# Kernel tuning notes

Hardware: AMD Instinct MI355X
Metric: run time of the kernel (lower is better)

## Reference

```python
import jax, jax.numpy as jnp
import numpy as np
import math

N, C, T, V = 8, 256, 128, 25
H, HC = 8, 32            # num_heads, head_channels
W, DIL = 3, 1            # window, dilation
O = 256                  # out_channels
PAD = (W + (W - 1) * (DIL - 1) - 1) // 2
B, L = N * T, W * V


def _ln(x, g, b):
    m = jnp.mean(x, -1, keepdims=True)
    v = jnp.var(x, -1, keepdims=True)
    return (x - m) * jax.lax.rsqrt(v + 1e-5) * g + b


def setup_inputs() -> dict:
    key = jax.random.key(0)
    ks = iter(jax.random.split(key, 40))
    def w(shape):
        return jax.random.normal(next(ks), shape, jnp.float32) * 0.02
    d = {"x": jax.random.normal(next(ks), (N, C, T, V), jnp.float32)}
    d.update(
        ln1_g=jnp.ones((C,)), ln1_b=jnp.zeros((C,)),
        Wq=w((C, C)), bq=jnp.zeros((C,)), Wqa=w((C, H)), bqa=jnp.zeros((H,)),
        Wk=w((C, C)), bk=jnp.zeros((C,)), Wka=w((C, H)), bka=jnp.zeros((H,)),
        Wv=w((C, C)), bv=jnp.zeros((C,)), Wt=w((C, C)), bt=jnp.zeros((C,)),
        Wp=w((C, C)), bp=jnp.zeros((C,)),
        ffn_g=jnp.ones((C,)), ffn_b=jnp.zeros((C,)),
        W1=w((C, C)), b1=jnp.zeros((C,)), W2=w((C, C)), b2=jnp.zeros((C,)),
        tn_g=jnp.ones((C,)), tn_b=jnp.zeros((C,)),
        c1_w=w((C, O)), c1_b=jnp.zeros((O,)),
        c2_w=w((W, O, O)), c2_b=jnp.zeros((O,)),
    )
    return d


def reference(x, ln1_g, ln1_b, Wq, bq, Wqa, bqa, Wk, bk, Wka, bka, Wv, bv,
              Wt, bt, Wp, bp, ffn_g, ffn_b, W1, b1, W2, b2, tn_g, tn_b,
              c1_w, c1_b, c2_w, c2_b):
    scale = 1.0 / math.sqrt(HC)
    # ---- Unfold over time: build window of frames around each t (nn.Unfold) ----
    xp = jnp.pad(x, ((0, 0), (0, 0), (PAD, PAD), (0, 0)))
    win = jnp.stack([jax.lax.dynamic_slice_in_dim(xp, k * DIL, T, 2) for k in range(W)], 2)  # (N,C,W,T,V)
    seq = win.transpose(0, 3, 2, 4, 1).reshape(B, L, C)  # (N*T, W*V, C)

    sep = lambda z: z.reshape(B, L, H, HC).transpose(0, 2, 1, 3)  # (B,H,L,HC)
    grp = lambda z: z.transpose(0, 2, 1, 3).reshape(B, -1, C)

    # ---- SpatioTemporalAttention (eval: dropouts off) ----
    nx = _ln(seq, ln1_g, ln1_b)
    q = nx @ Wq + bq                                            # (B,L,C)
    qw = jax.nn.softmax((q @ Wqa + bqa).transpose(0, 2, 1) * scale, axis=-1)  # (B,H,L)
    pq = jnp.einsum('bhl,bhlc->bhc', qw, sep(q)).reshape(B, 1, C)             # pooled query
    keys = nx @ Wk + bk
    kw = jax.nn.softmax(((keys * pq) @ Wka + bka).transpose(0, 2, 1) * scale, axis=-1)
    pk = jnp.einsum('bhl,bhlc->bhc', kw, sep(keys))             # pooled key (B,H,HC)
    vals = sep(nx @ Wv + bv)
    kv = grp(vals * pk[:, :, None, :]) @ Wt + bt                # (B,L,C)
    attn = (kv + q) @ Wp + bp                                   # residual-in-heads == plain add

    # ---- AttentionBranch residual + FFN ----
    att = attn + seq
    f = _ln(att, ffn_g, ffn_b)
    y = jax.nn.gelu(f @ W1 + b1, approximate=False) @ W2 + b2 + att  # (B,L,C)

    # ---- temporal branch: LN -> regroup frames -> 1x1 conv -> GELU -> (W,1) conv stride W ----
    t5 = _ln(y, tn_g, tn_b).reshape(N, T, W, V, C)
    h = jax.nn.gelu(t5 @ c1_w + c1_b, approximate=False)        # (N,T,W,V,O)
    out = jnp.einsum('ntwvi,wio->ntvo', h, c2_w) + c2_b         # stride==kernel conv == window contraction
    return out.transpose(0, 3, 1, 2)                            # (N,O,T,V)
```

## Files before the change

### kernel.cpp

```cpp
#include <hip/hip_runtime.h>


#define DI __device__ __forceinline__

constexpr int CC   = 256;
constexpr int CL   = 75;
constexpr int CV   = 25;
constexpr int CT   = 128;
constexpr int TP   = 130;
constexpr int MPAD = 8 * TP * CV;
constexpr int MBL  = 1024 * CL;
constexpr int MOUT = 8 * CT * CV;
constexpr float SM_SCALE = 0.17677669529663687f;

typedef __bf16 bf16x8 __attribute__((ext_vector_type(8)));
typedef float f32x4 __attribute__((ext_vector_type(4)));

DI float bf2f(unsigned short u) { return __uint_as_float(((unsigned)u) << 16); }
DI float bf2f_lo(unsigned u) { return __uint_as_float(u << 16); }
DI float bf2f_hi(unsigned u) { return __uint_as_float(u & 0xffff0000u); }
DI unsigned short f2bf(float f) {
  unsigned u = __float_as_uint(f);
  u += 0x7fffu + ((u >> 16) & 1u);
  return (unsigned short)(u >> 16);
}
DI unsigned packbf(float a, float b) {
  return (unsigned)f2bf(a) | ((unsigned)f2bf(b) << 16);
}
DI float geluf(float x) { return 0.5f * x * (1.f + erff(x * 0.70710678118654752440f)); }

DI void gll16(const unsigned short* g, unsigned short* l) {
  __builtin_amdgcn_global_load_lds(
      (const __attribute__((address_space(1))) unsigned int*)g,
      (__attribute__((address_space(3))) unsigned int*)l, 16, 0, 0);
}

DI int arow(int r) {
  int b = r / CL;
  int l = r - b * CL;
  int w = l / CV;
  int v = l - w * CV;
  int t = b & (CT - 1);
  int n = b >> 7;
  return (n * TP + t + w) * CV + v;
}

__global__ __launch_bounds__(256) void k_transpose(const float* __restrict__ x,
                                                   unsigned short* __restrict__ xtp) {
  __shared__ float tile[32][33];
  const int n = blockIdx.z;
  const int c0 = blockIdx.x * 32;
  const int tv0 = blockIdx.y * 32;
  const int tx = threadIdx.x & 31, ty = threadIdx.x >> 5;
#pragma unroll
  for (int j = 0; j < 32; j += 8) {
    tile[ty + j][tx] = x[((size_t)(n * CC + c0 + ty + j)) * 3200 + tv0 + tx];
  }
  __syncthreads();
#pragma unroll
  for (int j = 0; j < 32; j += 8) {
    int tv = tv0 + ty + j;
    int st = tv / CV, v = tv - st * CV;
    size_t row = ((size_t)n * TP + st + 1) * CV + v;
    xtp[row * CC + c0 + tx] = f2bf(tile[tx][ty + j]);
  }
}

__global__ __launch_bounds__(256) void k_zero_pad(unsigned short* __restrict__ xtp) {
  int i = blockIdx.x * 256 + threadIdx.x;
  int c = i & 255;
  int rid = i >> 8;
  int n = rid / 50;
  int rem = rid - n * 50;
  int side = rem / 25;
  int v = rem - side * 25;
  size_t row = ((size_t)n * TP + side * (TP - 1)) * CV + v;
  xtp[row * CC + c] = 0;
}

struct TJobs {
  const float* src[10];
  unsigned short* dst[10];
  int stride[10];
  int off[10];
};
__global__ __launch_bounds__(256) void k_wtrans(TJobs J) {
  __shared__ float tile[32][33];
  const int j = blockIdx.z;
  const float* src = J.src[j];
  unsigned short* dst = J.dst[j];
  const int stride = J.stride[j], off = J.off[j];
  const int k0 = blockIdx.x * 32, n0 = blockIdx.y * 32;
  const int tx = threadIdx.x & 31, ty = threadIdx.x >> 5;
#pragma unroll
  for (int jj = 0; jj < 32; jj += 8)
    tile[ty + jj][tx] = src[(size_t)(k0 + ty + jj) * 256 + n0 + tx];
  __syncthreads();
#pragma unroll
  for (int jj = 0; jj < 32; jj += 8)
    dst[(size_t)(n0 + ty + jj) * stride + off + k0 + tx] = f2bf(tile[tx][ty + jj]);
}

__global__ __launch_bounds__(256) void k_wtwp(const float* __restrict__ Wt,
                                              const float* __restrict__ Wp,
                                              unsigned short* __restrict__ fused) {
  __shared__ float wrow[256];
  const int k = blockIdx.x, n = threadIdx.x;
  wrow[n] = Wt[(size_t)k * 256 + n];
  __syncthreads();
  float acc = 0.f;
  for (int j = 0; j < 256; ++j) acc = fmaf(wrow[j], Wp[(size_t)j * 256 + n], acc);
  fused[(size_t)n * 512 + k] = f2bf(acc);
}

__global__ __launch_bounds__(256) void k_bias2(const float* __restrict__ bt,
                                               const float* __restrict__ Wp,
                                               const float* __restrict__ bp,
                                               const float* __restrict__ bq,
                                               const float* __restrict__ bk,
                                               const float* __restrict__ bv,
                                               float* __restrict__ bias2,
                                               float* __restrict__ bias3) {
  const int n = threadIdx.x;
  float acc = bp[n];
  for (int j = 0; j < 256; ++j) acc = fmaf(bt[j], Wp[(size_t)j * 256 + n], acc);
  bias2[n] = acc;
  bias3[n] = bq[n];
  bias3[256 + n] = bk[n];
  bias3[512 + n] = bv[n];
}

__global__ __launch_bounds__(256) void k_ln4(const unsigned short* __restrict__ X,
                                             const float* __restrict__ g,
                                             const float* __restrict__ b,
                                             unsigned short* __restrict__ Y) {
  const int row = blockIdx.x * 4 + (threadIdx.x >> 6);
  const int lane = threadIdx.x & 63;
  const uint2 u = *(const uint2*)(X + (size_t)row * CC + lane * 4);
  const float x0 = bf2f_lo(u.x), x1 = bf2f_hi(u.x), x2 = bf2f_lo(u.y), x3 = bf2f_hi(u.y);
  float s = x0 + x1 + x2 + x3;
  float q = x0 * x0 + x1 * x1 + x2 * x2 + x3 * x3;
#pragma unroll
  for (int o = 32; o; o >>= 1) { s += __shfl_xor(s, o); q += __shfl_xor(q, o); }
  const float mean = s * (1.f / CC);
  const float var = q * (1.f / CC) - mean * mean;
  const float rs = rsqrtf(var + 1e-5f);
  const float4 g4 = *(const float4*)(g + lane * 4);
  const float4 b4 = *(const float4*)(b + lane * 4);
  uint2 o2;
  o2.x = packbf((x0 - mean) * rs * g4.x + b4.x, (x1 - mean) * rs * g4.y + b4.y);
  o2.y = packbf((x2 - mean) * rs * g4.z + b4.z, (x3 - mean) * rs * g4.w + b4.w);
  *(uint2*)(Y + (size_t)row * CC + lane * 4) = o2;
}

template <int AMODE, int EPI, int KD, bool MULTI>
__global__ __launch_bounds__(512) void k_mgemm(const unsigned short* __restrict__ A,
                                               const unsigned short* __restrict__ BwT,
                                               const float* __restrict__ bias,
                                               unsigned short* __restrict__ Cout,
                                               float* __restrict__ FOut,
                                               int M) {
  if constexpr (MULTI) {
    const int z = blockIdx.y;
    BwT += (size_t)z * (256 * 256);
    bias += z * 256;
    Cout += (size_t)z * MPAD * CC;
  }
  __shared__ unsigned short SH[20480];
  const int tid = threadIdx.x;
  const int lane = tid & 63;
  const int wid = tid >> 6;
  const int wm = wid >> 2, wn = wid & 3;
  const int r0 = blockIdx.x * 64;
  f32x4 acc[2][4] = {};

  const bool sa = tid < 256;
  const int rA = r0 + (tid >> 2);
  const int seg8 = (tid & 3) * 8;
  const bool valid = sa && (rA < M);
  int hrb = 0;
  if (valid && AMODE == 4) {
    const int nb = rA / 3200, rr = rA - nb * 3200;
    const int tq = rr / 25, vq = rr - tq * 25;
    hrb = (nb * CT + tq) * CL + vq;
  }

  auto loadA4 = [&](int k0) -> uint4 {
    uint4 u = make_uint4(0, 0, 0, 0);
    if (!valid) return u;
    const int w = k0 >> 8;
    u = *(const uint4*)(A + (size_t)(hrb + w * CV) * CC + (k0 & 255) + seg8);
    return u;
  };
  auto stageB = [&](int buf, int k0) {
    unsigned short* bs = SH + 4096 + buf * 8192;
#pragma unroll
    for (int pp = 0; pp < 2; ++pp) {
      const int s = tid + pp * 512;
      gll16(BwT + (size_t)(s >> 2) * KD + k0 + (s & 3) * 8, bs + s * 8);
    }
  };
  auto stageAg = [&](int buf, int k0) {
    if (valid) gll16(A + (size_t)rA * CC + k0 + seg8, SH + buf * 2048 + tid * 8);
  };

  stageB(0, 0);
  if constexpr (AMODE == 0) {
    stageAg(0, 0);
  } else {
    const uint4 a0 = loadA4(0);
    if (sa) *(uint4*)(SH + tid * 8) = a0;
  }
  __syncthreads();

  constexpr int NT = KD / 32;
  int cur = 0;
  for (int t = 0; t < NT; ++t) {
    const int nxt = cur ^ 1;
    const bool more = (t + 1 < NT);
    uint4 an;
    if (more) {
      stageB(nxt, (t + 1) * 32);
      if constexpr (AMODE == 0) stageAg(nxt, (t + 1) * 32);
      else an = loadA4((t + 1) * 32);
    }
    const unsigned short* as = SH + cur * 2048;
    const unsigned short* bs = SH + 4096 + cur * 8192;
    bf16x8 af[2], bfr[4];
#pragma unroll
    for (int mi = 0; mi < 2; ++mi)
      af[mi] = *(const bf16x8*)(as + (wm * 32 + mi * 16 + (lane & 15)) * 32 + (lane >> 4) * 8);
#pragma unroll
    for (int ni = 0; ni < 4; ++ni)
      bfr[ni] = *(const bf16x8*)(bs + (wn * 64 + ni * 16 + (lane & 15)) * 32 + (lane >> 4) * 8);
#pragma unroll
    for (int mi = 0; mi < 2; ++mi)
#pragma unroll
      for (int ni = 0; ni < 4; ++ni)
        acc[mi][ni] = __builtin_amdgcn_mfma_f32_16x16x32_bf16(af[mi], bfr[ni], acc[mi][ni], 0, 0, 0);
    if (more) {
      if constexpr (AMODE != 0) {
        if (sa) *(uint4*)(SH + nxt * 2048 + tid * 8) = an;
      }
      __syncthreads();
      cur = nxt;
    }
  }

  const int ln15 = lane & 15, lq = lane >> 4;
  if constexpr (EPI == 4) {
#pragma unroll
    for (int mi = 0; mi < 2; ++mi) {
#pragma unroll
      for (int ni = 0; ni < 4; ++ni) {
        const int col = wn * 64 + ni * 16 + ln15;
        const float bcol = bias[col];
        const int rbase = r0 + wm * 32 + mi * 16 + lq * 4;
        const int nb = rbase / 3200, rr = rbase - nb * 3200;
        float4 v;
        v.x = acc[mi][ni][0] + bcol;
        v.y = acc[mi][ni][1] + bcol;
        v.z = acc[mi][ni][2] + bcol;
        v.w = acc[mi][ni][3] + bcol;
        *(float4*)(FOut + (size_t)nb * 819200 + (size_t)col * 3200 + rr) = v;
      }
    }
  } else {
    constexpr int LDC = 260;
    __syncthreads();
#pragma unroll
    for (int mi = 0; mi < 2; ++mi) {
#pragma unroll
      for (int ni = 0; ni < 4; ++ni) {
        const int col = wn * 64 + ni * 16 + ln15;
        const float bcol = bias[col];
#pragma unroll
        for (int rg = 0; rg < 4; ++rg) {
          const int lrow = wm * 32 + mi * 16 + lq * 4 + rg;
          SH[lrow * LDC + col] = f2bf(acc[mi][ni][rg] + bcol);
        }
      }
    }
    __syncthreads();
#pragma unroll
    for (int i = 0; i < 4; ++i) {
      const int idx = tid + i * 512;
      const int row = idx >> 5, ch = idx & 31;
      const int gr = r0 + row;
      if (gr < M)
        *(uint4*)(Cout + (size_t)gr * CC + ch * 8) = *(const uint4*)&SH[row * LDC + ch * 8];
    }
  }
}

__global__ __launch_bounds__(512) void k_chain(
    const unsigned short* __restrict__ VP, const unsigned short* __restrict__ QP,
    const float* __restrict__ PK, const unsigned short* __restrict__ XTP,
    const unsigned short* __restrict__ fusedB, const float* __restrict__ bias2,
    const unsigned short* __restrict__ W1T, const float* __restrict__ b1,
    const unsigned short* __restrict__ W2T, const float* __restrict__ b2,
    const float* __restrict__ ffn_g, const float* __restrict__ ffn_b,
    const unsigned short* __restrict__ c1wT, const float* __restrict__ c1b,
    const float* __restrict__ tn_g, const float* __restrict__ tn_b,
    unsigned short* __restrict__ Hout) {
  constexpr int LDC = 264;
  __shared__ unsigned short SH[16896 + 4096 + 16384];
  unsigned short* ACT = SH;
  unsigned short* AS = SH + 16896;
  unsigned short* BS = SH + 16896 + 4096;
  const int tid = threadIdx.x;
  const int lane = tid & 63, wid = tid >> 6;
  const int wm = wid >> 2, wn = wid & 3;
  const int ln15 = lane & 15, lq = lane >> 4;
  const int r0 = blockIdx.x * 64;

  const bool sa = tid < 256;
  const int rA = r0 + (tid >> 2);
  const int seg8 = (tid & 3) * 8;
  int ar = 0, bb = 0;
  if (sa) { ar = arow(rA); bb = rA / CL; }

  auto stageB = [&](const unsigned short* BwT, int KD, int buf, int k0) {
    unsigned short* bs = BS + buf * 8192;
#pragma unroll
    for (int pp = 0; pp < 2; ++pp) {
      const int s = tid + pp * 512;
      gll16(BwT + (size_t)(s >> 2) * KD + k0 + (s & 3) * 8, bs + s * 8);
    }
  };
  auto loadA5 = [&](int k0) -> uint4 {
    uint4 u = make_uint4(0, 0, 0, 0);
    if (!sa) return u;
    if (k0 < 256) {
      const int kg = k0 + seg8;
      const uint4 t4 = *(const uint4*)(VP + (size_t)ar * CC + kg);
      const float* sv = PK + bb * CC + kg;
      const float4 s0 = *(const float4*)sv;
      const float4 s1 = *(const float4*)(sv + 4);
      u.x = packbf(bf2f_lo(t4.x) * s0.x, bf2f_hi(t4.x) * s0.y);
      u.y = packbf(bf2f_lo(t4.y) * s0.z, bf2f_hi(t4.y) * s0.w);
      u.z = packbf(bf2f_lo(t4.z) * s1.x, bf2f_hi(t4.z) * s1.y);
      u.w = packbf(bf2f_lo(t4.w) * s1.z, bf2f_hi(t4.w) * s1.w);
    } else {
      u = *(const uint4*)(QP + (size_t)ar * CC + (k0 - 256) + seg8);
    }
    return u;
  };
  auto ln_inplace = [&](const float* g, const float* b) {
    const float4 g4 = *(const float4*)(g + lane * 4);
    const float4 b4 = *(const float4*)(b + lane * 4);
#pragma unroll
    for (int rr = 0; rr < 8; ++rr) {
      const int row = wid * 8 + rr;
      const uint2 u = *(const uint2*)(ACT + row * LDC + lane * 4);
      const float x0 = bf2f_lo(u.x), x1 = bf2f_hi(u.x);
      const float x2 = bf2f_lo(u.y), x3 = bf2f_hi(u.y);
      float s = x0 + x1 + x2 + x3;
      float q = x0 * x0 + x1 * x1 + x2 * x2 + x3 * x3;
#pragma unroll
      for (int o = 32; o; o >>= 1) { s += __shfl_xor(s, o); q += __shfl_xor(q, o); }
      const float mean = s * (1.f / CC);
      const float var = q * (1.f / CC) - mean * mean;
      const float rs = rsqrtf(var + 1e-5f);
      uint2 o2;
      o2.x = packbf((x0 - mean) * rs * g4.x + b4.x, (x1 - mean) * rs * g4.y + b4.y);
      o2.y = packbf((x2 - mean) * rs * g4.z + b4.z, (x3 - mean) * rs * g4.w + b4.w);
      *(uint2*)(ACT + row * LDC + lane * 4) = o2;
    }
  };
  auto gemmACT = [&](const unsigned short* BwT, f32x4 (&a)[2][4]) {
    int c2 = 0;
    for (int t = 0; t < 8; ++t) {
      if (t + 1 < 8) stageB(BwT, 256, c2 ^ 1, (t + 1) * 32);
      bf16x8 af[2], bfr[4];
#pragma unroll
      for (int mi = 0; mi < 2; ++mi)
        af[mi] = *(const bf16x8*)(ACT + (wm * 32 + mi * 16 + ln15) * LDC + t * 32 + lq * 8);
#pragma unroll
      for (int ni = 0; ni < 4; ++ni)
        bfr[ni] = *(const bf16x8*)(BS + c2 * 8192 + (wn * 64 + ni * 16 + ln15) * 32 + lq * 8);
#pragma unroll
      for (int mi = 0; mi < 2; ++mi)
#pragma unroll
        for (int ni = 0; ni < 4; ++ni)
          a[mi][ni] = __builtin_amdgcn_mfma_f32_16x16x32_bf16(af[mi], bfr[ni], a[mi][ni], 0, 0, 0);
      if (t + 1 < 8) { __syncthreads(); c2 ^= 1; }
    }
  };

  f32x4 acc[2][4] = {};
  stageB(fusedB, 512, 0, 0);
  { uint4 a0 = loadA5(0); if (sa) *(uint4*)(AS + tid * 8) = a0; }
  __syncthreads();
  int cur = 0;
  for (int t = 0; t < 16; ++t) {
    const int nxt = cur ^ 1;
    const bool more = (t + 1 < 16);
    uint4 an;
    if (more) { stageB(fusedB, 512, nxt, (t + 1) * 32); an = loadA5((t + 1) * 32); }
    bf16x8 af[2], bfr[4];
#pragma unroll
    for (int mi = 0; mi < 2; ++mi)
      af[mi] = *(const bf16x8*)(AS + cur * 2048 + (wm * 32 + mi * 16 + ln15) * 32 + lq * 8);
#pragma unroll
    for (int ni = 0; ni < 4; ++ni)
      bfr[ni] = *(const bf16x8*)(BS + cur * 8192 + (wn * 64 + ni * 16 + ln15) * 32 + lq * 8);
#pragma unroll
    for (int mi = 0; mi < 2; ++mi)
#pragma unroll
      for (int ni = 0; ni < 4; ++ni)
        acc[mi][ni] = __builtin_amdgcn_mfma_f32_16x16x32_bf16(af[mi], bfr[ni], acc[mi][ni], 0, 0, 0);
    if (more) {
      if (sa) *(uint4*)(AS + nxt * 2048 + tid * 8) = an;
      __syncthreads();
      cur = nxt;
    }
  }
  f32x4 attres[2][4];
#pragma unroll
  for (int mi = 0; mi < 2; ++mi) {
#pragma unroll
    for (int ni = 0; ni < 4; ++ni) {
      const int col = wn * 64 + ni * 16 + ln15;
      const float bcol = bias2[col];
#pragma unroll
      for (int rg = 0; rg < 4; ++rg) {
        const int r = r0 + wm * 32 + mi * 16 + lq * 4 + rg;
        attres[mi][ni][rg] = acc[mi][ni][rg] + bcol + bf2f(XTP[(size_t)arow(r) * CC + col]);
      }
    }
  }
  stageB(W1T, 256, 0, 0);
#pragma unroll
  for (int mi = 0; mi < 2; ++mi)
#pragma unroll
    for (int ni = 0; ni < 4; ++ni) {
      const int col = wn * 64 + ni * 16 + ln15;
#pragma unroll
      for (int rg = 0; rg < 4; ++rg)
        ACT[(wm * 32 + mi * 16 + lq * 4 + rg) * LDC + col] = f2bf(attres[mi][ni][rg]);
    }
  __syncthreads();
  ln_inplace(ffn_g, ffn_b);
  __syncthreads();

  f32x4 acc2[2][4] = {};
  gemmACT(W1T, acc2);
  stageB(W2T, 256, 0, 0);
  __syncthreads();
#pragma unroll
  for (int mi = 0; mi < 2; ++mi)
#pragma unroll
    for (int ni = 0; ni < 4; ++ni) {
      const int col = wn * 64 + ni * 16 + ln15;
      const float bcol = b1[col];
#pragma unroll
      for (int rg = 0; rg < 4; ++rg)
        ACT[(wm * 32 + mi * 16 + lq * 4 + rg) * LDC + col] = f2bf(geluf(acc2[mi][ni][rg] + bcol));
    }
  __syncthreads();

  f32x4 acc3[2][4] = {};
  gemmACT(W2T, acc3);
  stageB(c1wT, 256, 0, 0);
  __syncthreads();
#pragma unroll
  for (int mi = 0; mi < 2; ++mi)
#pragma unroll
    for (int ni = 0; ni < 4; ++ni) {
      const int col = wn * 64 + ni * 16 + ln15;
      const float bcol = b2[col];
#pragma unroll
      for (int rg = 0; rg < 4; ++rg)
        ACT[(wm * 32 + mi * 16 + lq * 4 + rg) * LDC + col] =
            f2bf(acc3[mi][ni][rg] + bcol + attres[mi][ni][rg]);
    }
  __syncthreads();
  ln_inplace(tn_g, tn_b);
  __syncthreads();

  f32x4 acc4[2][4] = {};
  gemmACT(c1wT, acc4);
  __syncthreads();
#pragma unroll
  for (int mi = 0; mi < 2; ++mi)
#pragma unroll
    for (int ni = 0; ni < 4; ++ni) {
      const int col = wn * 64 + ni * 16 + ln15;
      const float bcol = c1b[col];
#pragma unroll
      for (int rg = 0; rg < 4; ++rg)
        ACT[(wm * 32 + mi * 16 + lq * 4 + rg) * LDC + col] = f2bf(geluf(acc4[mi][ni][rg] + bcol));
    }
  __syncthreads();
#pragma unroll
  for (int i = 0; i < 4; ++i) {
    const int idx = tid + i * 512;
    const int row = idx >> 5, ch = idx & 31;
    *(uint4*)(Hout + (size_t)(r0 + row) * CC + ch * 8) = *(const uint4*)&ACT[row * LDC + ch * 8];
  }
}

__global__ __launch_bounds__(256) void k_proj8(const unsigned short* __restrict__ SRC,
                                               const float* __restrict__ Wsm,
                                               const float* __restrict__ bsm,
                                               float* __restrict__ OUT) {
  const int r = blockIdx.x * 4 + (threadIdx.x >> 6);
  const int lane = threadIdx.x & 63;
  const int c = lane * 4;
  const uint2 u = *(const uint2*)(SRC + (size_t)r * CC + c);
  const float m0 = bf2f_lo(u.x), m1 = bf2f_hi(u.x), m2 = bf2f_lo(u.y), m3 = bf2f_hi(u.y);
  float p[8] = {};
#pragma unroll
  for (int j = 0; j < 4; ++j) {
    const float mj = (j == 0) ? m0 : (j == 1) ? m1 : (j == 2) ? m2 : m3;
#pragma unroll
    for (int h = 0; h < 8; ++h) p[h] += mj * Wsm[(c + j) * 8 + h];
  }
#pragma unroll
  for (int h = 0; h < 8; ++h) {
#pragma unroll
    for (int o = 32; o; o >>= 1) p[h] += __shfl_down(p[h], o);
  }
  if (lane == 0) {
#pragma unroll
    for (int h = 0; h < 8; ++h) OUT[(size_t)r * 8 + h] = p[h] + bsm[h];
  }
}

template <int SIDE>
__global__ __launch_bounds__(256) void k_attpool(const unsigned short* __restrict__ ROWS,
                                                 const float* __restrict__ QA,
                                                 const float* __restrict__ PQ,
                                                 const float* __restrict__ Wka,
                                                 const float* __restrict__ bka,
                                                 float* __restrict__ OUT) {
  __shared__ unsigned short rows[CL * CC];
  __shared__ float uu[(SIDE == 1) ? 8 * 258 : 8];
  __shared__ float lg[8 * 76];
  __shared__ float inv8[8];
  __shared__ int arl[CL];
  const int b = blockIdx.x;
  const int t = threadIdx.x;

  if (t < CL) arl[t] = arow(b * CL + t);
  __syncthreads();

  for (int i = t; i < CL * 32; i += 256) {
    const int r = i >> 5, seg = i & 31;
    gll16(ROWS + (size_t)arl[r] * CC + seg * 8, &rows[i * 8]);
  }
  if constexpr (SIDE == 0) {
    for (int i = t; i < CL * 2; i += 256) {
      const int l = i >> 1, q = i & 1;
      const float4 v = *(const float4*)(QA + (size_t)arl[l] * 8 + q * 4);
      lg[(q * 4 + 0) * 76 + l] = v.x * SM_SCALE;
      lg[(q * 4 + 1) * 76 + l] = v.y * SM_SCALE;
      lg[(q * 4 + 2) * 76 + l] = v.z * SM_SCALE;
      lg[(q * 4 + 3) * 76 + l] = v.w * SM_SCALE;
    }
  } else {
    for (int i = t; i < CC * 8; i += 256) {
      const int c = i >> 3, h = i & 7;
      uu[h * 258 + c] = PQ[(size_t)b * CC + c] * Wka[c * 8 + h];
    }
  }
  __syncthreads();

  if constexpr (SIDE == 1) {
    const int c0 = (t & 127) * 2;
    for (int i = t; i < CL * 8; i += 256) {
      const int h = i / CL, l = i - h * CL;
      float acc = bka[h];
#pragma unroll 4
      for (int jj = 0; jj < CC; jj += 2) {
        const int c = (c0 + jj) & 255;
        const unsigned pr = *(const unsigned*)&rows[l * CC + c];
        acc = fmaf(bf2f_lo(pr), uu[h * 258 + c], acc);
        acc = fmaf(bf2f_hi(pr), uu[h * 258 + c + 1], acc);
      }
      lg[h * 76 + l] = acc * SM_SCALE;
    }
    __syncthreads();
  }

  if (t < 8) {
    float m = -1e30f;
    for (int l = 0; l < CL; ++l) m = fmaxf(m, lg[t * 76 + l]);
    float s = 0.f;
    for (int l = 0; l < CL; ++l) {
      const float e = __expf(lg[t * 76 + l] - m);
      lg[t * 76 + l] = e;
      s += e;
    }
    inv8[t] = 1.f / s;
  }
  __syncthreads();

  {
    const int h = t >> 5;
    float acc = 0.f;
    for (int l = 0; l < CL; ++l) acc = fmaf(lg[h * 76 + l], bf2f(rows[l * CC + t]), acc);
    OUT[(size_t)b * CC + t] = acc * inv8[h];
  }
}

extern "C" void kernel_launch(void* const* d_in, const int* in_sizes, int n_in,
                              void* d_out, int out_size, void* d_ws, size_t ws_size,
                              hipStream_t stream) {
  const float* x = (const float*)d_in[0];
  const float* ln1_g = (const float*)d_in[1];
  const float* ln1_b = (const float*)d_in[2];
  const float* Wq = (const float*)d_in[3];
  const float* bq = (const float*)d_in[4];
  const float* Wqa = (const float*)d_in[5];
  const float* bqa = (const float*)d_in[6];
  const float* Wk = (const float*)d_in[7];
  const float* bk = (const float*)d_in[8];
  const float* Wka = (const float*)d_in[9];
  const float* bka = (const float*)d_in[10];
  const float* Wv = (const float*)d_in[11];
  const float* bv = (const float*)d_in[12];
  const float* Wt = (const float*)d_in[13];
  const float* bt = (const float*)d_in[14];
  const float* Wp = (const float*)d_in[15];
  const float* bp = (const float*)d_in[16];
  const float* ffn_g = (const float*)d_in[17];
  const float* ffn_b = (const float*)d_in[18];
  const float* W1 = (const float*)d_in[19];
  const float* b1 = (const float*)d_in[20];
  const float* W2 = (const float*)d_in[21];
  const float* b2 = (const float*)d_in[22];
  const float* tn_g = (const float*)d_in[23];
  const float* tn_b = (const float*)d_in[24];
  const float* c1w = (const float*)d_in[25];
  const float* c1b = (const float*)d_in[26];
  const float* c2w = (const float*)d_in[27];
  const float* c2b = (const float*)d_in[28];
  float* out = (float*)d_out;

  char* wp = (char*)d_ws;
  auto alloc = [&](size_t bytes) -> char* {
    char* p = wp;
    wp += (bytes + 255) & ~(size_t)255;
    return p;
  };
  unsigned short* XTP = (unsigned short*)alloc((size_t)MPAD * CC * 2);
  unsigned short* LNXP = (unsigned short*)alloc((size_t)MPAD * CC * 2);
  unsigned short* QKVP = (unsigned short*)alloc((size_t)3 * MPAD * CC * 2);
  unsigned short* QP = QKVP;
  unsigned short* KP = QKVP + (size_t)MPAD * CC;
  unsigned short* VP = QKVP + (size_t)2 * MPAD * CC;
  unsigned short* Hb = (unsigned short*)alloc((size_t)MBL * CC * 2);
  float* QA = (float*)alloc((size_t)MPAD * 8 * 4);
  float* PQ = (float*)alloc((size_t)1024 * CC * 4);
  float* PK = (float*)alloc((size_t)1024 * CC * 4);
  unsigned short* WqkvT = (unsigned short*)alloc((size_t)3 * 256 * 256 * 2);
  unsigned short* W1T = (unsigned short*)alloc(256 * 256 * 2);
  unsigned short* W2T = (unsigned short*)alloc(256 * 256 * 2);
  unsigned short* c1wT = (unsigned short*)alloc(256 * 256 * 2);
  unsigned short* c2wT = (unsigned short*)alloc(256 * 768 * 2);
  unsigned short* fusedB = (unsigned short*)alloc(256 * 512 * 2);
  float* bias2 = (float*)alloc(256 * 4);
  float* bias3 = (float*)alloc(768 * 4);

  TJobs J;
  const float* srcs[10] = {Wq, Wk, Wv, W1, W2, c1w, c2w, c2w + 65536, c2w + 131072, Wp};
  unsigned short* dsts[10] = {WqkvT, WqkvT + 65536, WqkvT + 131072, W1T, W2T, c1wT,
                              c2wT, c2wT, c2wT, fusedB};
  const int strides[10] = {256, 256, 256, 256, 256, 256, 768, 768, 768, 512};
  const int offs[10] = {0, 0, 0, 0, 0, 0, 0, 256, 512, 256};
  for (int i = 0; i < 10; ++i) {
    J.src[i] = srcs[i]; J.dst[i] = dsts[i]; J.stride[i] = strides[i]; J.off[i] = offs[i];
  }
  k_wtrans<<<dim3(8, 8, 10), 256, 0, stream>>>(J);
  k_wtwp<<<256, 256, 0, stream>>>(Wt, Wp, fusedB);
  k_bias2<<<1, 256, 0, stream>>>(bt, Wp, bp, bq, bk, bv, bias2, bias3);

  k_transpose<<<dim3(8, 100, 8), 256, 0, stream>>>(x, XTP);
  k_zero_pad<<<400, 256, 0, stream>>>(XTP);
  k_ln4<<<MPAD / 4, 256, 0, stream>>>(XTP, ln1_g, ln1_b, LNXP);

  const int gP = (MPAD + 63) / 64;
  const int gO = MOUT / 64;
  k_mgemm<0, 0, 256, true><<<dim3(gP, 3), 512, 0, stream>>>(
      LNXP, WqkvT, bias3, QKVP, nullptr, MPAD);

  k_proj8<<<MPAD / 4, 256, 0, stream>>>(QP, Wqa, bqa, QA);
  k_attpool<0><<<1024, 256, 0, stream>>>(QP, QA, nullptr, nullptr, nullptr, PQ);
  k_attpool<1><<<1024, 256, 0, stream>>>(KP, nullptr, PQ, Wka, bka, PK);

  k_chain<<<MBL / 64, 512, 0, stream>>>(VP, QP, PK, XTP, fusedB, bias2,
                                        W1T, b1, W2T, b2, ffn_g, ffn_b,
                                        c1wT, c1b, tn_g, tn_b, Hb);

  k_mgemm<4, 4, 768, false><<<gO, 512, 0, stream>>>(Hb, c2wT, c2b, nullptr, out, MOUT);
}
```

Before: 311.8 us.

## Fuse query head projection into attention pooling and tweak chain kernel epilogue

Removes the separate k_proj8 kernel and QA buffer by computing the query head logits (q @ Wqa + bqa) directly inside k_attpool<0>, using the same shared-memory dot-product path the key side already uses. In k_chain, the residual rows are precomputed into registers, the W1 staging is issued earlier, and the ACT store is merged into the residual loop. A launch-bounds occupancy hint of 4 is added. In exchange, attpool<0> now does redundant per-window projection work for overlapping padded rows, and the occupancy hint may force register spills.

Result: no change. 311.7 us (-0.0%).

```diff
diff --git a/kernel.cpp b/kernel.cpp
--- a/kernel.cpp
+++ b/kernel.cpp
@@ -293,7 +293,7 @@
   }
 }
 
-__global__ __launch_bounds__(512) void k_chain(
+__global__ __launch_bounds__(512, 4) void k_chain(
     const unsigned short* __restrict__ VP, const unsigned short* __restrict__ QP,
     const float* __restrict__ PK, const unsigned short* __restrict__ XTP,
     const unsigned short* __restrict__ fusedB, const float* __restrict__ bias2,
@@ -319,6 +319,10 @@
   const int seg8 = (tid & 3) * 8;
   int ar = 0, bb = 0;
   if (sa) { ar = arow(rA); bb = rA / CL; }
+  int xrow[8];
+#pragma unroll
+  for (int i = 0; i < 8; ++i)
+    xrow[i] = arow(r0 + wm * 32 + (i >> 2) * 16 + lq * 4 + (i & 3));
 
   auto stageB = [&](const unsigned short* BwT, int KD, int buf, int k0) {
     unsigned short* bs = BS + buf * 8192;
@@ -416,6 +420,7 @@
       cur = nxt;
     }
   }
+  stageB(W1T, 256, 0, 0);
   f32x4 attres[2][4];
 #pragma unroll
   for (int mi = 0; mi < 2; ++mi) {
@@ -425,21 +430,12 @@
       const float bcol = bias2[col];
 #pragma unroll
       for (int rg = 0; rg < 4; ++rg) {
-        const int r = r0 + wm * 32 + mi * 16 + lq * 4 + rg;
-        attres[mi][ni][rg] = acc[mi][ni][rg] + bcol + bf2f(XTP[(size_t)arow(r) * CC + col]);
+        attres[mi][ni][rg] =
+            acc[mi][ni][rg] + bcol + bf2f(XTP[(size_t)xrow[mi * 4 + rg] * CC + col]);
+        ACT[(wm * 32 + mi * 16 + lq * 4 + rg) * LDC + col] = f2bf(attres[mi][ni][rg]);
       }
     }
   }
-  stageB(W1T, 256, 0, 0);
-#pragma unroll
-  for (int mi = 0; mi < 2; ++mi)
-#pragma unroll
-    for (int ni = 0; ni < 4; ++ni) {
-      const int col = wn * 64 + ni * 16 + ln15;
-#pragma unroll
-      for (int rg = 0; rg < 4; ++rg)
-        ACT[(wm * 32 + mi * 16 + lq * 4 + rg) * LDC + col] = f2bf(attres[mi][ni][rg]);
-    }
   __syncthreads();
   ln_inplace(ffn_g, ffn_b);
   __syncthreads();
@@ -501,42 +497,14 @@
   }
 }
 
-__global__ __launch_bounds__(256) void k_proj8(const unsigned short* __restrict__ SRC,
-                                               const float* __restrict__ Wsm,
-                                               const float* __restrict__ bsm,
-                                               float* __restrict__ OUT) {
-  const int r = blockIdx.x * 4 + (threadIdx.x >> 6);
-  const int lane = threadIdx.x & 63;
-  const int c = lane * 4;
-  const uint2 u = *(const uint2*)(SRC + (size_t)r * CC + c);
-  const float m0 = bf2f_lo(u.x), m1 = bf2f_hi(u.x), m2 = bf2f_lo(u.y), m3 = bf2f_hi(u.y);
-  float p[8] = {};
-#pragma unroll
-  for (int j = 0; j < 4; ++j) {
-    const float mj = (j == 0) ? m0 : (j == 1) ? m1 : (j == 2) ? m2 : m3;
-#pragma unroll
-    for (int h = 0; h < 8; ++h) p[h] += mj * Wsm[(c + j) * 8 + h];
-  }
-#pragma unroll
-  for (int h = 0; h < 8; ++h) {
-#pragma unroll
-    for (int o = 32; o; o >>= 1) p[h] += __shfl_down(p[h], o);
-  }
-  if (lane == 0) {
-#pragma unroll
-    for (int h = 0; h < 8; ++h) OUT[(size_t)r * 8 + h] = p[h] + bsm[h];
-  }
-}
-
 template <int SIDE>
 __global__ __launch_bounds__(256) void k_attpool(const unsigned short* __restrict__ ROWS,
-                                                 const float* __restrict__ QA,
                                                  const float* __restrict__ PQ,
-                                                 const float* __restrict__ Wka,
-                                                 const float* __restrict__ bka,
+                                                 const float* __restrict__ W8,
+                                                 const float* __restrict__ b8,
                                                  float* __restrict__ OUT) {
   __shared__ unsigned short rows[CL * CC];
-  __shared__ float uu[(SIDE == 1) ? 8 * 258 : 8];
+  __shared__ float uu[8 * 258];
   __shared__ float lg[8 * 76];
   __shared__ float inv8[8];
   __shared__ int arl[CL];
@@ -550,28 +518,20 @@
     const int r = i >> 5, seg = i & 31;
     gll16(ROWS + (size_t)arl[r] * CC + seg * 8, &rows[i * 8]);
   }
-  if constexpr (SIDE == 0) {
-    for (int i = t; i < CL * 2; i += 256) {
-      const int l = i >> 1, q = i & 1;
-      const float4 v = *(const float4*)(QA + (size_t)arl[l] * 8 + q * 4);
-      lg[(q * 4 + 0) * 76 + l] = v.x * SM_SCALE;
-      lg[(q * 4 + 1) * 76 + l] = v.y * SM_SCALE;
-      lg[(q * 4 + 2) * 76 + l] = v.z * SM_SCALE;
-      lg[(q * 4 + 3) * 76 + l] = v.w * SM_SCALE;
-    }
-  } else {
-    for (int i = t; i < CC * 8; i += 256) {
-      const int c = i >> 3, h = i & 7;
-      uu[h * 258 + c] = PQ[(size_t)b * CC + c] * Wka[c * 8 + h];
-    }
-  }
-  __syncthreads();
-
-  if constexpr (SIDE == 1) {
+  for (int i = t; i < CC * 8; i += 256) {
+    const int c = i >> 3, h = i & 7;
+    if constexpr (SIDE == 0)
+      uu[h * 258 + c] = W8[c * 8 + h];
+    else
+      uu[h * 258 + c] = PQ[(size_t)b * CC + c] * W8[c * 8 + h];
+  }
+  __syncthreads();
+
+  {
     const int c0 = (t & 127) * 2;
     for (int i = t; i < CL * 8; i += 256) {
       const int h = i / CL, l = i - h * CL;
-      float acc = bka[h];
+      float acc = b8[h];
 #pragma unroll 4
       for (int jj = 0; jj < CC; jj += 2) {
         const int c = (c0 + jj) & 255;
@@ -581,8 +541,8 @@
       }
       lg[h * 76 + l] = acc * SM_SCALE;
     }
-    __syncthreads();
-  }
+  }
+  __syncthreads();
 
   if (t < 8) {
     float m = -1e30f;
@@ -652,7 +612,6 @@
   unsigned short* KP = QKVP + (size_t)MPAD * CC;
   unsigned short* VP = QKVP + (size_t)2 * MPAD * CC;
   unsigned short* Hb = (unsigned short*)alloc((size_t)MBL * CC * 2);
-  float* QA = (float*)alloc((size_t)MPAD * 8 * 4);
   float* PQ = (float*)alloc((size_t)1024 * CC * 4);
   float* PK = (float*)alloc((size_t)1024 * CC * 4);
   unsigned short* WqkvT = (unsigned short*)alloc((size_t)3 * 256 * 256 * 2);
@@ -686,9 +645,8 @@
   k_mgemm<0, 0, 256, true><<<dim3(gP, 3), 512, 0, stream>>>(
       LNXP, WqkvT, bias3, QKVP, nullptr, MPAD);
 
-  k_proj8<<<MPAD / 4, 256, 0, stream>>>(QP, Wqa, bqa, QA);
-  k_attpool<0><<<1024, 256, 0, stream>>>(QP, QA, nullptr, nullptr, nullptr, PQ);
-  k_attpool<1><<<1024, 256, 0, stream>>>(KP, nullptr, PQ, Wka, bka, PK);
+  k_attpool<0><<<1024, 256, 0, stream>>>(QP, nullptr, Wqa, bqa, PQ);
+  k_attpool<1><<<1024, 256, 0, stream>>>(KP, PQ, Wka, bka, PK);
 
   k_chain<<<MBL / 64, 512, 0, stream>>>(VP, QP, PK, XTP, fusedB, bias2,
                                         W1T, b1, W2T, b2, ffn_g, ffn_b,
```
